# Kernel tuning notes

Hardware: AMD Instinct MI355X
Metric: run time of the kernel (lower is better)

## Reference

```python
import jax, jax.numpy as jnp
import numpy as np

B, IN, OUT, Q = 2048, 1024, 1024, 16

def setup_inputs() -> dict:
    key = jax.random.key(0)
    k1, k2, k3, k4 = jax.random.split(key, 4)
    bound = 1.0 / np.sqrt(IN)
    x = jax.random.normal(k1, (B, IN), dtype=jnp.float32)
    indices = jax.random.randint(k2, (B, IN), 0, Q, dtype=jnp.int32)
    # param_index: per-(quantile, input-feature) weight vector of length size_out
    param_table = jax.random.uniform(k3, (Q, IN, OUT), dtype=jnp.float32,
                                     minval=-bound, maxval=bound)
    bias = jax.random.uniform(k4, (OUT,), dtype=jnp.float32,
                              minval=-bound, maxval=bound)
    return {"x": x, "indices": indices, "param_table": param_table,
            "bias": bias, "store_activations": 0, "get_indices": 0, "use_db": 0}

def reference(x, indices, param_table, bias, store_activations, get_indices, use_db):
    # out[b, o] = sum_i param_table[indices[b,i], i, o] * x[b,i]  + bias[o]
    # Expressed as Q masked matmuls to avoid a [B, IN, OUT] gathered intermediate:
    # route each (b, i) contribution to its quantile's weight slab.
    q = param_table.shape[0]
    onehot = jax.nn.one_hot(indices, q, dtype=x.dtype)      # [B, IN, Q]
    xq = onehot * x[..., None]                               # [B, IN, Q]
    w_times_x = jnp.einsum('biq,qio->bo', xq, param_table)   # [B, OUT]
    return w_times_x + bias
```

## Files before the change

### kernel.cpp

```cpp
#include <hip/hip_runtime.h>
#include <stdint.h>

#define B_SZ   2048
#define IN_SZ  1024
#define OUT_SZ 1024
#define Q_SZ   16
#define NZB    4

typedef __attribute__((ext_vector_type(8))) short short8;
typedef __attribute__((ext_vector_type(4))) float floatx4;
typedef __attribute__((ext_vector_type(2))) unsigned short u16x2;
typedef __attribute__((ext_vector_type(2))) short s16x2;

__device__ __forceinline__ unsigned short f32_to_bf16_rne(float f) {
    union { float f; uint32_t u; } v; v.f = f;
    uint32_t u = v.u;
    return (unsigned short)((u + 0x7FFFu + ((u >> 16) & 1u)) >> 16);
}

__device__ __forceinline__ uint32_t mask3(uint32_t xv, uint32_t ohv, unsigned short sh) {
    union { uint32_t u; u16x2 v; s16x2 s; } t;
    t.u = ohv;
    u16x2 shv; shv.x = sh; shv.y = sh;
    t.v = t.v << shv;
    s16x2 f15; f15.x = 15; f15.y = 15;
    t.s = t.s >> f15;
    return xv & t.u;
}

__device__ __forceinline__ void gload_lds16(const void* g, void* l) {
    __builtin_amdgcn_global_load_lds(
        (const __attribute__((address_space(1))) unsigned int*)g,
        (__attribute__((address_space(3))) unsigned int*)l, 16, 0, 0);
}

__global__ void k_build_wf(const float* __restrict__ W, unsigned short* __restrict__ Wf) {
    const int S = blockIdx.x;
    const int q = S & 15, ih = (S >> 4) & 3, xb = (S >> 6) & 7, zb = S >> 9;
    const int t = threadIdx.x;
    const int i0 = zb * 256 + ih * 64;
    const int o0 = xb * 128;
    __shared__ unsigned short lds[64][130];

#pragma unroll
    for (int it = 0; it < 8; ++it) {
        int r  = it * 8 + (t >> 5);
        int c4 = (t & 31) * 4;
        float4 v = *(const float4*)(W + ((size_t)(q * 1024 + i0 + r)) * 1024 + o0 + c4);
        unsigned short h0 = f32_to_bf16_rne(v.x), h1 = f32_to_bf16_rne(v.y);
        unsigned short h2 = f32_to_bf16_rne(v.z), h3 = f32_to_bf16_rne(v.w);
        *(uint32_t*)&lds[r][c4]     = (uint32_t)h0 | ((uint32_t)h1 << 16);
        *(uint32_t*)&lds[r][c4 + 2] = (uint32_t)h2 | ((uint32_t)h3 << 16);
    }
    __syncthreads();

    unsigned short* dst = Wf + (size_t)S * 8192;
#pragma unroll
    for (int it = 0; it < 4; ++it) {
        int c = it * 256 + t;
        int L = c & 63;
        int hnt = c >> 6;
        int h = hnt >> 3, nt = hnt & 7;
        int ol = nt * 16 + (L & 15);
        int il = h * 32 + (L >> 4) * 8;
        unsigned short v[8];
#pragma unroll
        for (int j = 0; j < 8; ++j) v[j] = lds[il + j][ol];
        *(uint4*)(dst + (size_t)c * 8) = *(uint4*)v;
    }
}

__global__ __launch_bounds__(256, 2) void k_gemm(const unsigned short* __restrict__ Wf,
                                                 const float* __restrict__ x,
                                                 const int* __restrict__ idx,
                                                 float* __restrict__ P) {
    const int tid  = threadIdx.x;
    const int wave = tid >> 6, lane = tid & 63;

    const int id = blockIdx.x;
    const int zb = id & 3;
    const int xb = (id >> 2) & 7;
    const int yb = id >> 5;
    const int o0 = xb * 128, b0 = yb * 128, ibase = zb * 256;

    const char* wbase = (const char*)Wf + (size_t)(zb * 8 + xb) * 64 * 16384;
    const int   lofs  = lane * 16;

    __shared__ unsigned char sm[2][16384];

    const int arow = b0 + wave * 32 + (lane & 15);
    const float* xg = x + (size_t)arow * IN_SZ + ibase + (lane >> 4) * 8;
    const int*   ig = idx + (size_t)arow * IN_SZ + ibase + (lane >> 4) * 8;

    floatx4 acc[16];
#pragma unroll
    for (int i = 0; i < 16; ++i) acc[i] = (floatx4){0.f, 0.f, 0.f, 0.f};

    uint4 xr[2][2], oh[2][2];

#define RELOADA(ih)                                                           \
    {   int io_ = (ih) * 64;                                                  \
        _Pragma("unroll")                                                     \
        for (int mt_ = 0; mt_ < 2; ++mt_)                                     \
            _Pragma("unroll")                                                 \
            for (int hh_ = 0; hh_ < 2; ++hh_) {                               \
                const float* xp_ = xg + mt_ * 16 * IN_SZ + io_ + hh_ * 32;    \
                const int*   ip_ = ig + mt_ * 16 * IN_SZ + io_ + hh_ * 32;    \
                float a_[8]; int b_[8];                                       \
                *(float4*)(a_)     = *(const float4*)xp_;                     \
                *(float4*)(a_ + 4) = *((const float4*)xp_ + 1);               \
                *(int4*)(b_)       = *(const int4*)ip_;                       \
                *(int4*)(b_ + 4)   = *((const int4*)ip_ + 1);                 \
                unsigned short xv_[8];                                        \
                _Pragma("unroll")                                             \
                for (int j_ = 0; j_ < 8; ++j_) xv_[j_] = f32_to_bf16_rne(a_[j_]); \
                xr[mt_][hh_] = *(uint4*)xv_;                                  \
                uint32_t iw_[4];                                              \
                _Pragma("unroll")                                             \
                for (int w_ = 0; w_ < 4; ++w_)                                \
                    iw_[w_] = (1u << b_[2 * w_]) | ((1u << b_[2 * w_ + 1]) << 16); \
                oh[mt_][hh_] = *(uint4*)iw_;                                  \
            }                                                                 \
    }

#define MASKS(hh)                                                             \
        _Pragma("unroll")                                                     \
        for (int mt_ = 0; mt_ < 2; ++mt_) {                                   \
            aF[mt_].u.x = mask3(xr[mt_][hh].x, oh[mt_][hh].x, sh_);           \
            aF[mt_].u.y = mask3(xr[mt_][hh].y, oh[mt_][hh].y, sh_);           \
            aF[mt_].u.z = mask3(xr[mt_][hh].z, oh[mt_][hh].z, sh_);           \
            aF[mt_].u.w = mask3(xr[mt_][hh].w, oh[mt_][hh].w, sh_);           \
        }

    const int soff = wave * 4096 + lofs;
#define STAGE(s_, pb_)                                                        \
    {   const char* gp_ = wbase + (size_t)(s_) * 16384 + soff;                \
        unsigned char* lp_ = &sm[pb_][soff];                                  \
        gload_lds16(gp_,        lp_);                                         \
        gload_lds16(gp_ + 1024, lp_ + 1024);                                  \
        gload_lds16(gp_ + 2048, lp_ + 2048);                                  \
        gload_lds16(gp_ + 3072, lp_ + 3072);                                  \
    }

#define SLAB(s_, pc_, pn_)                                                    \
    {   if ((s_) < 63) STAGE((s_) + 1, pn_);                                  \
        if ((s_) && (((s_) & 15) == 0)) RELOADA((s_) >> 4);                   \
        const unsigned short sh_ = (unsigned short)(15 - ((s_) & 15));        \
        union { uint4 u; short8 s8; } aF[2];                                  \
        short8 f_[8];                                                         \
        _Pragma("unroll")                                                     \
        for (int nt_ = 0; nt_ < 8; ++nt_)                                     \
            f_[nt_] = *(const short8*)&sm[pc_][nt_ * 1024 + lofs];            \
        MASKS(0);                                                             \
        _Pragma("unroll")                                                     \
        for (int mt_ = 0; mt_ < 2; ++mt_)                                     \
            _Pragma("unroll")                                                 \
            for (int nt_ = 0; nt_ < 8; ++nt_)                                 \
                acc[mt_ * 8 + nt_] = __builtin_amdgcn_mfma_f32_16x16x32_bf16( \
                    aF[mt_].s8, f_[nt_], acc[mt_ * 8 + nt_], 0, 0, 0);        \
        _Pragma("unroll")                                                     \
        for (int nt_ = 0; nt_ < 8; ++nt_)                                     \
            f_[nt_] = *(const short8*)&sm[pc_][8192 + nt_ * 1024 + lofs];     \
        MASKS(1);                                                             \
        _Pragma("unroll")                                                     \
        for (int mt_ = 0; mt_ < 2; ++mt_)                                     \
            _Pragma("unroll")                                                 \
            for (int nt_ = 0; nt_ < 8; ++nt_)                                 \
                acc[mt_ * 8 + nt_] = __builtin_amdgcn_mfma_f32_16x16x32_bf16( \
                    aF[mt_].s8, f_[nt_], acc[mt_ * 8 + nt_], 0, 0, 0);        \
        __syncthreads();                                                      \
    }

    RELOADA(0);
    STAGE(0, 0);
    __syncthreads();

#pragma unroll 1
    for (int g = 0; g < 32; ++g) {
        SLAB(2 * g,     0, 1);
        SLAB(2 * g + 1, 1, 0);
    }

    float* Pz = P + (size_t)zb * (B_SZ * OUT_SZ);
    int cn = lane & 15, rq = lane >> 4;
#pragma unroll
    for (int mt = 0; mt < 2; ++mt)
#pragma unroll
        for (int nt = 0; nt < 8; ++nt) {
            int bb = b0 + wave * 32 + mt * 16 + rq * 4;
            int oo = o0 + nt * 16 + cn;
#pragma unroll
            for (int e = 0; e < 4; ++e)
                Pz[(size_t)(bb + e) * OUT_SZ + oo] = acc[mt * 8 + nt][e];
        }
#undef RELOADA
#undef MASKS
#undef STAGE
#undef SLAB
}

__global__ void k_reduce(const float* __restrict__ P, const float* __restrict__ bias,
                         float* __restrict__ out) {
    int t = blockIdx.x * 256 + threadIdx.x;
    const float4* b4 = (const float4*)bias;
    float4 a = b4[t & 255];
#pragma unroll
    for (int z = 0; z < NZB; ++z) {
        float4 v = ((const float4*)P)[(size_t)z * (B_SZ * OUT_SZ / 4) + t];
        a.x += v.x; a.y += v.y; a.z += v.z; a.w += v.w;
    }
    ((float4*)out)[t] = a;
}

__global__ void k_naive(const float* __restrict__ x, const int* __restrict__ idx,
                        const float* __restrict__ W, const float* __restrict__ bias,
                        float* __restrict__ out) {
    int b = blockIdx.x;
    int o = threadIdx.x * 4;
    float4 acc = *(const float4*)(bias + o);
    const float* xr = x + (size_t)b * IN_SZ;
    const int*   ir = idx + (size_t)b * IN_SZ;
    for (int i = 0; i < IN_SZ; ++i) {
        float xv = xr[i];
        int q = ir[i];
        float4 w4 = *(const float4*)(W + ((size_t)q * IN_SZ + i) * OUT_SZ + o);
        acc.x += xv * w4.x; acc.y += xv * w4.y;
        acc.z += xv * w4.z; acc.w += xv * w4.w;
    }
    *(float4*)(out + (size_t)b * OUT_SZ + o) = acc;
}

extern "C" void kernel_launch(void* const* d_in, const int* in_sizes, int n_in,
                              void* d_out, int out_size, void* d_ws, size_t ws_size,
                              hipStream_t stream) {
    const float* x    = (const float*)d_in[0];
    const int*   idx  = (const int*)d_in[1];
    const float* W    = (const float*)d_in[2];
    const float* bias = (const float*)d_in[3];
    float* out = (float*)d_out;

    const size_t wf_bytes = (size_t)2048 * 16384;
    const size_t p_bytes  = (size_t)NZB * B_SZ * OUT_SZ * 4;
    if (ws_size < wf_bytes + p_bytes) {
        k_naive<<<dim3(B_SZ), dim3(256), 0, stream>>>(x, idx, W, bias, out);
        return;
    }
    unsigned short* Wf = (unsigned short*)d_ws;
    float* P = (float*)((char*)d_ws + wf_bytes);

    k_build_wf<<<dim3(2048), dim3(256), 0, stream>>>(W, Wf);
    k_gemm<<<dim3(NZB * 8 * (B_SZ / 128)), dim3(256), 0, stream>>>(Wf, x, idx, P);
    k_reduce<<<dim3(2048), dim3(256), 0, stream>>>(P, bias, out);
}
```

Baseline: 192.1 us.

## Deepen LDS weight pipeline to four stages with manual vmcnt waits and prefetched A loads

Moves the weight-slab staging from a double buffer to a four-slot ring in LDS, loading three slabs ahead and splitting each stage into two halves that are issued between the MFMA halves. Replaces __syncthreads with explicit s_waitcnt vmcnt counts and raw s_barrier, and raises wave priority around the MFMA blocks. The x/index loads for the next 64-column chunk are now issued two slabs early and converted later, so their global latency is hidden. In exchange it doubles LDS use per block, which may cut occupancy under launch_bounds(256,2), and relies on hand-counted vmcnt values that must stay exact for correctness.

```diff
diff --git a/kernel.cpp b/kernel.cpp
--- a/kernel.cpp
+++ b/kernel.cpp
@@ -34,6 +34,8 @@
         (__attribute__((address_space(3))) unsigned int*)l, 16, 0, 0);
 }
 
+#define VM(n) asm volatile("s_waitcnt vmcnt(" #n ")" ::: "memory")
+
 __global__ void k_build_wf(const float* __restrict__ W, unsigned short* __restrict__ Wf) {
     const int S = blockIdx.x;
     const int q = S & 15, ih = (S >> 4) & 3, xb = (S >> 6) & 7, zb = S >> 9;
@@ -86,7 +88,7 @@
     const char* wbase = (const char*)Wf + (size_t)(zb * 8 + xb) * 64 * 16384;
     const int   lofs  = lane * 16;
 
-    __shared__ unsigned char sm[2][16384];
+    __shared__ unsigned char sm[4][16384];
 
     const int arow = b0 + wave * 32 + (lane & 15);
     const float* xg = x + (size_t)arow * IN_SZ + ibase + (lane >> 4) * 8;
@@ -97,20 +99,33 @@
     for (int i = 0; i < 16; ++i) acc[i] = (floatx4){0.f, 0.f, 0.f, 0.f};
 
     uint4 xr[2][2], oh[2][2];
-
-#define RELOADA(ih)                                                           \
-    {   int io_ = (ih) * 64;                                                  \
-        _Pragma("unroll")                                                     \
+    float4 xA[2][2][2];
+    int4   iA[2][2][2];
+
+#define ISSUE_XLD(ih_)                                                        \
+    {   _Pragma("unroll")                                                     \
         for (int mt_ = 0; mt_ < 2; ++mt_)                                     \
             _Pragma("unroll")                                                 \
             for (int hh_ = 0; hh_ < 2; ++hh_) {                               \
-                const float* xp_ = xg + mt_ * 16 * IN_SZ + io_ + hh_ * 32;    \
-                const int*   ip_ = ig + mt_ * 16 * IN_SZ + io_ + hh_ * 32;    \
+                const float* xp_ = xg + mt_ * 16 * IN_SZ + (ih_) * 64 + hh_ * 32; \
+                const int*   ip_ = ig + mt_ * 16 * IN_SZ + (ih_) * 64 + hh_ * 32; \
+                xA[mt_][hh_][0] = *(const float4*)xp_;                        \
+                xA[mt_][hh_][1] = *((const float4*)xp_ + 1);                  \
+                iA[mt_][hh_][0] = *(const int4*)ip_;                          \
+                iA[mt_][hh_][1] = *((const int4*)ip_ + 1);                    \
+            }                                                                 \
+    }
+
+#define CONVERT()                                                             \
+    {   _Pragma("unroll")                                                     \
+        for (int mt_ = 0; mt_ < 2; ++mt_)                                     \
+            _Pragma("unroll")                                                 \
+            for (int hh_ = 0; hh_ < 2; ++hh_) {                               \
                 float a_[8]; int b_[8];                                       \
-                *(float4*)(a_)     = *(const float4*)xp_;                     \
-                *(float4*)(a_ + 4) = *((const float4*)xp_ + 1);               \
-                *(int4*)(b_)       = *(const int4*)ip_;                       \
-                *(int4*)(b_ + 4)   = *((const int4*)ip_ + 1);                 \
+                *(float4*)a_       = xA[mt_][hh_][0];                         \
+                *(float4*)(a_ + 4) = xA[mt_][hh_][1];                         \
+                *(int4*)b_         = iA[mt_][hh_][0];                         \
+                *(int4*)(b_ + 4)   = iA[mt_][hh_][1];                         \
                 unsigned short xv_[8];                                        \
                 _Pragma("unroll")                                             \
                 for (int j_ = 0; j_ < 8; ++j_) xv_[j_] = f32_to_bf16_rne(a_[j_]); \
@@ -132,53 +147,83 @@
             aF[mt_].u.w = mask3(xr[mt_][hh].w, oh[mt_][hh].w, sh_);           \
         }
 
-    const int soff = wave * 4096 + lofs;
-#define STAGE(s_, pb_)                                                        \
-    {   const char* gp_ = wbase + (size_t)(s_) * 16384 + soff;                \
-        unsigned char* lp_ = &sm[pb_][soff];                                  \
+#define STAGE2(s_, r_, h_)                                                    \
+    {   const int off_ = (h_) * 8192 + wave * 2048 + lofs;                    \
+        const char* gp_ = wbase + (size_t)(s_) * 16384 + off_;                \
+        unsigned char* lp_ = (unsigned char*)sm + (r_) * 16384 + off_;        \
+        gload_lds16(gp_,        lp_);                                         \
+        gload_lds16(gp_ + 1024, lp_ + 1024);                                  \
+    }
+
+#define STAGE4(s_, r_)                                                        \
+    {   const int off_ = wave * 4096 + lofs;                                  \
+        const char* gp_ = wbase + (size_t)(s_) * 16384 + off_;                \
+        unsigned char* lp_ = (unsigned char*)sm + (r_) * 16384 + off_;        \
         gload_lds16(gp_,        lp_);                                         \
         gload_lds16(gp_ + 1024, lp_ + 1024);                                  \
         gload_lds16(gp_ + 2048, lp_ + 2048);                                  \
         gload_lds16(gp_ + 3072, lp_ + 3072);                                  \
     }
 
-#define SLAB(s_, pc_, pn_)                                                    \
-    {   if ((s_) < 63) STAGE((s_) + 1, pn_);                                  \
-        if ((s_) && (((s_) & 15) == 0)) RELOADA((s_) >> 4);                   \
-        const unsigned short sh_ = (unsigned short)(15 - ((s_) & 15));        \
-        union { uint4 u; short8 s8; } aF[2];                                  \
-        short8 f_[8];                                                         \
-        _Pragma("unroll")                                                     \
-        for (int nt_ = 0; nt_ < 8; ++nt_)                                     \
-            f_[nt_] = *(const short8*)&sm[pc_][nt_ * 1024 + lofs];            \
-        MASKS(0);                                                             \
+#define MFMA16(fa)                                                            \
         _Pragma("unroll")                                                     \
         for (int mt_ = 0; mt_ < 2; ++mt_)                                     \
             _Pragma("unroll")                                                 \
             for (int nt_ = 0; nt_ < 8; ++nt_)                                 \
                 acc[mt_ * 8 + nt_] = __builtin_amdgcn_mfma_f32_16x16x32_bf16( \
-                    aF[mt_].s8, f_[nt_], acc[mt_ * 8 + nt_], 0, 0, 0);        \
-        _Pragma("unroll")                                                     \
-        for (int nt_ = 0; nt_ < 8; ++nt_)                                     \
-            f_[nt_] = *(const short8*)&sm[pc_][8192 + nt_ * 1024 + lofs];     \
-        MASKS(1);                                                             \
-        _Pragma("unroll")                                                     \
-        for (int mt_ = 0; mt_ < 2; ++mt_)                                     \
-            _Pragma("unroll")                                                 \
-            for (int nt_ = 0; nt_ < 8; ++nt_)                                 \
-                acc[mt_ * 8 + nt_] = __builtin_amdgcn_mfma_f32_16x16x32_bf16( \
-                    aF[mt_].s8, f_[nt_], acc[mt_ * 8 + nt_], 0, 0, 0);        \
-        __syncthreads();                                                      \
-    }
-
-    RELOADA(0);
-    STAGE(0, 0);
-    __syncthreads();
+                    aF[mt_].s8, (fa)[nt_], acc[mt_ * 8 + nt_], 0, 0, 0);
+
+    ISSUE_XLD(0);
+    CONVERT();
+    STAGE4(0, 0);
+    STAGE4(1, 1);
+    STAGE4(2, 2);
+    VM(8);
+    __builtin_amdgcn_s_barrier();
 
 #pragma unroll 1
-    for (int g = 0; g < 32; ++g) {
-        SLAB(2 * g,     0, 1);
-        SLAB(2 * g + 1, 1, 0);
+    for (int s = 0; s < 64; ++s) {
+        if (s && (s & 15) == 0) CONVERT();
+        const int rc = s & 3, rn = (s + 3) & 3;
+        const unsigned short sh_ = (unsigned short)(15 - (s & 15));
+        union { uint4 u; short8 s8; } aF[2];
+        short8 f[8];
+
+        {
+            const unsigned char* bp = (const unsigned char*)sm + rc * 16384 + lofs;
+#pragma unroll
+            for (int nt = 0; nt < 8; ++nt) f[nt] = *(const short8*)(bp + nt * 1024);
+            if (s < 61) STAGE2(s + 3, rn, 0);
+            MASKS(0);
+            __builtin_amdgcn_s_barrier();
+            __builtin_amdgcn_sched_barrier(0);
+            __builtin_amdgcn_s_setprio(1);
+            MFMA16(f);
+            __builtin_amdgcn_s_setprio(0);
+            __builtin_amdgcn_sched_barrier(0);
+            __builtin_amdgcn_s_barrier();
+        }
+
+        {
+            const unsigned char* bp = (const unsigned char*)sm + rc * 16384 + 8192 + lofs;
+#pragma unroll
+            for (int nt = 0; nt < 8; ++nt) f[nt] = *(const short8*)(bp + nt * 1024);
+            if (s < 61) STAGE2(s + 3, rn, 1);
+            if ((s & 15) == 14 && s < 48) ISSUE_XLD((s >> 4) + 1);
+            MASKS(1);
+            if (s == 61)      { VM(4); }
+            else if (s == 62) { VM(0); }
+            else if (s == 63) {  }
+            else if ((s & 15) == 14 || (s & 15) == 15) { VM(24); }
+            else              { VM(8); }
+            __builtin_amdgcn_s_barrier();
+            __builtin_amdgcn_sched_barrier(0);
+            __builtin_amdgcn_s_setprio(1);
+            MFMA16(f);
+            __builtin_amdgcn_s_setprio(0);
+            __builtin_amdgcn_sched_barrier(0);
+            __builtin_amdgcn_s_barrier();
+        }
     }
 
     float* Pz = P + (size_t)zb * (B_SZ * OUT_SZ);
@@ -193,10 +238,12 @@
             for (int e = 0; e < 4; ++e)
                 Pz[(size_t)(bb + e) * OUT_SZ + oo] = acc[mt * 8 + nt][e];
         }
-#undef RELOADA
+#undef ISSUE_XLD
+#undef CONVERT
 #undef MASKS
-#undef STAGE
-#undef SLAB
+#undef STAGE2
+#undef STAGE4
+#undef MFMA16
 }
 
 __global__ void k_reduce(const float* __restrict__ P, const float* __restrict__ bias,
```

Measured after the change: 193.5 us. About the same (+0.7%).

## Switch wave tiling from 4x1 to 2x2 with 64x64 per-wave tiles

Applied to the files above, without the earlier changes.

Each wave now computes a 64x64 output tile (4 M-subtiles by 4 N-subtiles) in a 2x2 wave grid instead of a 32x128 strip. Each wave reads half as much B fragment data from LDS per slab. In exchange, every wave holds and masks twice as many A rows, so A global loads, bf16 conversion and one-hot mask work are duplicated across the two column waves. Register pressure also rises. The unrolled two-slab macro is replaced by a rolled single-slab loop with the buffer index computed at runtime.

```diff
diff --git a/kernel.cpp b/kernel.cpp
--- a/kernel.cpp
+++ b/kernel.cpp
@@ -76,6 +76,7 @@
                                                  float* __restrict__ P) {
     const int tid  = threadIdx.x;
     const int wave = tid >> 6, lane = tid & 63;
+    const int wr = wave >> 1, wc = wave & 1;
 
     const int id = blockIdx.x;
     const int zb = id & 3;
@@ -88,7 +89,7 @@
 
     __shared__ unsigned char sm[2][16384];
 
-    const int arow = b0 + wave * 32 + (lane & 15);
+    const int arow = b0 + wr * 64 + (lane & 15);
     const float* xg = x + (size_t)arow * IN_SZ + ibase + (lane >> 4) * 8;
     const int*   ig = idx + (size_t)arow * IN_SZ + ibase + (lane >> 4) * 8;
 
@@ -96,12 +97,12 @@
 #pragma unroll
     for (int i = 0; i < 16; ++i) acc[i] = (floatx4){0.f, 0.f, 0.f, 0.f};
 
-    uint4 xr[2][2], oh[2][2];
+    uint4 xr[4][2], oh[4][2];
 
 #define RELOADA(ih)                                                           \
     {   int io_ = (ih) * 64;                                                  \
         _Pragma("unroll")                                                     \
-        for (int mt_ = 0; mt_ < 2; ++mt_)                                     \
+        for (int mt_ = 0; mt_ < 4; ++mt_)                                     \
             _Pragma("unroll")                                                 \
             for (int hh_ = 0; hh_ < 2; ++hh_) {                               \
                 const float* xp_ = xg + mt_ * 16 * IN_SZ + io_ + hh_ * 32;    \
@@ -125,7 +126,7 @@
 
 #define MASKS(hh)                                                             \
         _Pragma("unroll")                                                     \
-        for (int mt_ = 0; mt_ < 2; ++mt_) {                                   \
+        for (int mt_ = 0; mt_ < 4; ++mt_) {                                   \
             aF[mt_].u.x = mask3(xr[mt_][hh].x, oh[mt_][hh].x, sh_);           \
             aF[mt_].u.y = mask3(xr[mt_][hh].y, oh[mt_][hh].y, sh_);           \
             aF[mt_].u.z = mask3(xr[mt_][hh].z, oh[mt_][hh].z, sh_);           \
@@ -142,61 +143,59 @@
         gload_lds16(gp_ + 3072, lp_ + 3072);                                  \
     }
 
-#define SLAB(s_, pc_, pn_)                                                    \
-    {   if ((s_) < 63) STAGE((s_) + 1, pn_);                                  \
-        if ((s_) && (((s_) & 15) == 0)) RELOADA((s_) >> 4);                   \
-        const unsigned short sh_ = (unsigned short)(15 - ((s_) & 15));        \
-        union { uint4 u; short8 s8; } aF[2];                                  \
-        short8 f_[8];                                                         \
-        _Pragma("unroll")                                                     \
-        for (int nt_ = 0; nt_ < 8; ++nt_)                                     \
-            f_[nt_] = *(const short8*)&sm[pc_][nt_ * 1024 + lofs];            \
-        MASKS(0);                                                             \
-        _Pragma("unroll")                                                     \
-        for (int mt_ = 0; mt_ < 2; ++mt_)                                     \
-            _Pragma("unroll")                                                 \
-            for (int nt_ = 0; nt_ < 8; ++nt_)                                 \
-                acc[mt_ * 8 + nt_] = __builtin_amdgcn_mfma_f32_16x16x32_bf16( \
-                    aF[mt_].s8, f_[nt_], acc[mt_ * 8 + nt_], 0, 0, 0);        \
-        _Pragma("unroll")                                                     \
-        for (int nt_ = 0; nt_ < 8; ++nt_)                                     \
-            f_[nt_] = *(const short8*)&sm[pc_][8192 + nt_ * 1024 + lofs];     \
-        MASKS(1);                                                             \
-        _Pragma("unroll")                                                     \
-        for (int mt_ = 0; mt_ < 2; ++mt_)                                     \
-            _Pragma("unroll")                                                 \
-            for (int nt_ = 0; nt_ < 8; ++nt_)                                 \
-                acc[mt_ * 8 + nt_] = __builtin_amdgcn_mfma_f32_16x16x32_bf16( \
-                    aF[mt_].s8, f_[nt_], acc[mt_ * 8 + nt_], 0, 0, 0);        \
-        __syncthreads();                                                      \
-    }
-
     RELOADA(0);
     STAGE(0, 0);
     __syncthreads();
 
 #pragma unroll 1
-    for (int g = 0; g < 32; ++g) {
-        SLAB(2 * g,     0, 1);
-        SLAB(2 * g + 1, 1, 0);
+    for (int s = 0; s < 64; ++s) {
+        const int rc = s & 1;
+        if (s < 63) STAGE(s + 1, rc ^ 1);
+        if (s && (s & 15) == 0) RELOADA(s >> 4);
+        const unsigned short sh_ = (unsigned short)(15 - (s & 15));
+        union { uint4 u; short8 s8; } aF[4];
+
+        const unsigned char* bp = &sm[rc][wc * 4096 + lofs];
+        short8 f0[4], f1[4];
+#pragma unroll
+        for (int nt = 0; nt < 4; ++nt) f0[nt] = *(const short8*)(bp + nt * 1024);
+#pragma unroll
+        for (int nt = 0; nt < 4; ++nt) f1[nt] = *(const short8*)(bp + 8192 + nt * 1024);
+
+        MASKS(0);
+#pragma unroll
+        for (int mt = 0; mt < 4; ++mt)
+#pragma unroll
+            for (int nt = 0; nt < 4; ++nt)
+                acc[mt * 4 + nt] = __builtin_amdgcn_mfma_f32_16x16x32_bf16(
+                    aF[mt].s8, f0[nt], acc[mt * 4 + nt], 0, 0, 0);
+
+        MASKS(1);
+#pragma unroll
+        for (int mt = 0; mt < 4; ++mt)
+#pragma unroll
+            for (int nt = 0; nt < 4; ++nt)
+                acc[mt * 4 + nt] = __builtin_amdgcn_mfma_f32_16x16x32_bf16(
+                    aF[mt].s8, f1[nt], acc[mt * 4 + nt], 0, 0, 0);
+
+        __syncthreads();
     }
 
     float* Pz = P + (size_t)zb * (B_SZ * OUT_SZ);
     int cn = lane & 15, rq = lane >> 4;
 #pragma unroll
-    for (int mt = 0; mt < 2; ++mt)
-#pragma unroll
-        for (int nt = 0; nt < 8; ++nt) {
-            int bb = b0 + wave * 32 + mt * 16 + rq * 4;
-            int oo = o0 + nt * 16 + cn;
+    for (int mt = 0; mt < 4; ++mt)
+#pragma unroll
+        for (int nt = 0; nt < 4; ++nt) {
+            int bb = b0 + wr * 64 + mt * 16 + rq * 4;
+            int oo = o0 + wc * 64 + nt * 16 + cn;
 #pragma unroll
             for (int e = 0; e < 4; ++e)
-                Pz[(size_t)(bb + e) * OUT_SZ + oo] = acc[mt * 8 + nt][e];
+                Pz[(size_t)(bb + e) * OUT_SZ + oo] = acc[mt * 4 + nt][e];
         }
 #undef RELOADA
 #undef MASKS
 #undef STAGE
-#undef SLAB
 }
 
 __global__ void k_reduce(const float* __restrict__ P, const float* __restrict__ bias,
```

New measurement: 210.7 us. 1.1x slower.

## Deepen LDS ring to four slabs and double-buffer weight fragments in registers

Applied to the files above, without the earlier changes.

The shared-memory weight ring grows from two to four 16KB slabs, so global-to-LDS loads are issued two slabs ahead instead of one. Weight fragments are also double-buffered in registers: the next slab's first half is read from LDS while the current MFMAs run. The main loop is unrolled by four, and the activation reload moves to the top of each group. The aim is to hide global and LDS latency behind MFMA work, at the cost of 64KB of LDS per block and more VGPRs, which could squeeze the two-blocks-per-CU occupancy.

```diff
diff --git a/kernel.cpp b/kernel.cpp
--- a/kernel.cpp
+++ b/kernel.cpp
@@ -86,7 +86,7 @@
     const char* wbase = (const char*)Wf + (size_t)(zb * 8 + xb) * 64 * 16384;
     const int   lofs  = lane * 16;
 
-    __shared__ unsigned char sm[2][16384];
+    __shared__ unsigned char sm[4][16384];
 
     const int arow = b0 + wave * 32 + (lane & 15);
     const float* xg = x + (size_t)arow * IN_SZ + ibase + (lane >> 4) * 8;
@@ -97,6 +97,7 @@
     for (int i = 0; i < 16; ++i) acc[i] = (floatx4){0.f, 0.f, 0.f, 0.f};
 
     uint4 xr[2][2], oh[2][2];
+    short8 fc[8], fn[8];
 
 #define RELOADA(ih)                                                           \
     {   int io_ = (ih) * 64;                                                  \
@@ -133,52 +134,58 @@
         }
 
     const int soff = wave * 4096 + lofs;
-#define STAGE(s_, pb_)                                                        \
+#define STAGE(s_, r_)                                                         \
     {   const char* gp_ = wbase + (size_t)(s_) * 16384 + soff;                \
-        unsigned char* lp_ = &sm[pb_][soff];                                  \
+        unsigned char* lp_ = (unsigned char*)sm + (r_) * 16384 + soff;        \
         gload_lds16(gp_,        lp_);                                         \
         gload_lds16(gp_ + 1024, lp_ + 1024);                                  \
         gload_lds16(gp_ + 2048, lp_ + 2048);                                  \
         gload_lds16(gp_ + 3072, lp_ + 3072);                                  \
     }
 
-#define SLAB(s_, pc_, pn_)                                                    \
-    {   if ((s_) < 63) STAGE((s_) + 1, pn_);                                  \
-        if ((s_) && (((s_) & 15) == 0)) RELOADA((s_) >> 4);                   \
-        const unsigned short sh_ = (unsigned short)(15 - ((s_) & 15));        \
-        union { uint4 u; short8 s8; } aF[2];                                  \
-        short8 f_[8];                                                         \
+#define DSREAD(dst, rr, hofs)                                                 \
+    {   const unsigned char* bp_ = (const unsigned char*)sm + (rr) * 16384 +  \
+                                   (hofs) + lofs;                             \
         _Pragma("unroll")                                                     \
         for (int nt_ = 0; nt_ < 8; ++nt_)                                     \
-            f_[nt_] = *(const short8*)&sm[pc_][nt_ * 1024 + lofs];            \
-        MASKS(0);                                                             \
+            (dst)[nt_] = *(const short8*)(bp_ + nt_ * 1024);                  \
+    }
+
+#define MFMA16(fa)                                                            \
         _Pragma("unroll")                                                     \
         for (int mt_ = 0; mt_ < 2; ++mt_)                                     \
             _Pragma("unroll")                                                 \
             for (int nt_ = 0; nt_ < 8; ++nt_)                                 \
                 acc[mt_ * 8 + nt_] = __builtin_amdgcn_mfma_f32_16x16x32_bf16( \
-                    aF[mt_].s8, f_[nt_], acc[mt_ * 8 + nt_], 0, 0, 0);        \
-        _Pragma("unroll")                                                     \
-        for (int nt_ = 0; nt_ < 8; ++nt_)                                     \
-            f_[nt_] = *(const short8*)&sm[pc_][8192 + nt_ * 1024 + lofs];     \
+                    aF[mt_].s8, (fa)[nt_], acc[mt_ * 8 + nt_], 0, 0, 0);
+
+#define SLAB(s_, rc_, rn_, rs_)                                               \
+    {   if ((s_) < 62) STAGE((s_) + 2, rs_);                                  \
+        DSREAD(fn, rc_, 8192);                                                \
+        const unsigned short sh_ = (unsigned short)(15 - ((s_) & 15));        \
+        union { uint4 u; short8 s8; } aF[2];                                  \
+        MASKS(0);                                                             \
+        MFMA16(fc);                                                           \
+        if ((s_) < 63) DSREAD(fc, rn_, 0);                                    \
         MASKS(1);                                                             \
-        _Pragma("unroll")                                                     \
-        for (int mt_ = 0; mt_ < 2; ++mt_)                                     \
-            _Pragma("unroll")                                                 \
-            for (int nt_ = 0; nt_ < 8; ++nt_)                                 \
-                acc[mt_ * 8 + nt_] = __builtin_amdgcn_mfma_f32_16x16x32_bf16( \
-                    aF[mt_].s8, f_[nt_], acc[mt_ * 8 + nt_], 0, 0, 0);        \
+        MFMA16(fn);                                                           \
         __syncthreads();                                                      \
     }
 
     RELOADA(0);
     STAGE(0, 0);
+    STAGE(1, 1);
     __syncthreads();
+    DSREAD(fc, 0, 0);
 
 #pragma unroll 1
-    for (int g = 0; g < 32; ++g) {
-        SLAB(2 * g,     0, 1);
-        SLAB(2 * g + 1, 1, 0);
+    for (int gg = 0; gg < 16; ++gg) {
+        if (gg && (gg & 3) == 0) RELOADA(gg >> 2);
+        const int s0 = gg * 4;
+        SLAB(s0 + 0, 0, 1, 2);
+        SLAB(s0 + 1, 1, 2, 3);
+        SLAB(s0 + 2, 2, 3, 0);
+        SLAB(s0 + 3, 3, 0, 1);
     }
 
     float* Pz = P + (size_t)zb * (B_SZ * OUT_SZ);
@@ -196,6 +203,8 @@
 #undef RELOADA
 #undef MASKS
 #undef STAGE
+#undef DSREAD
+#undef MFMA16
 #undef SLAB
 }
 
```

Result: no change. 191.4 us (-0.4%).
